# Optimization experiments

Hardware: AMD Instinct MI355X
Metric: run time of the kernel (lower is better)

## Reference

```python
import jax, jax.numpy as jnp
import numpy as np

THETA = 10000.0

def precompute_freqs_cis(dim, seq_len):
    freqs = 1.0 / THETA ** (jnp.arange(0, dim, 2)[: dim // 2].astype(jnp.float32) / dim)
    t = jnp.arange(seq_len, dtype=jnp.float32)
    ang = jnp.outer(t, freqs)  # [T, dim/2]
    return jax.lax.complex(jnp.cos(ang), jnp.sin(ang))

def apply_rope(x, freqs_cis):
    # x: [..., T, D]; freqs_cis: [T, D/2] complex
    xr = x.astype(jnp.float32).reshape(*x.shape[:-1], -1, 2)
    xc = jax.lax.complex(xr[..., 0], xr[..., 1]) * freqs_cis
    out = jnp.stack([jnp.real(xc), jnp.imag(xc)], axis=-1).reshape(x.shape)
    return out.astype(x.dtype)

def setup_inputs() -> dict:
    key = jax.random.key(0)
    k1, k2, k3, k4 = jax.random.split(key, 4)
    B, T, E, DQ, DV = 4, 2048, 1024, 128, 128
    s = 1.0 / np.sqrt(E)
    return {
        "embedding_word": jax.random.normal(k1, (B, T, E), dtype=jnp.float32),
        "w_Q": jax.random.normal(k2, (DQ, E), dtype=jnp.float32) * s,  # torch Linear weight [out,in]
        "w_K": jax.random.normal(k3, (DQ, E), dtype=jnp.float32) * s,
        "w_V": jax.random.normal(k4, (DV, E), dtype=jnp.float32) * s,
    }

def reference(embedding_word, w_Q, w_K, w_V):
    T = embedding_word.shape[-2]
    dq = w_Q.shape[0]
    q = jnp.einsum("bte,de->btd", embedding_word, w_Q)
    k = jnp.einsum("bte,de->btd", embedding_word, w_K)
    v = jnp.einsum("bte,de->btd", embedding_word, w_V)
    fc = precompute_freqs_cis(dq, T)
    q = apply_rope(q, fc)
    k = apply_rope(k, fc)
    scores = jnp.einsum("bqd,bkd->bqk", q, k)
    causal = jnp.triu(jnp.ones((T, T), dtype=bool), k=1)
    masked = jnp.where(causal, -jnp.inf, scores)
    weights = jax.nn.softmax(masked / jnp.sqrt(jnp.float32(dq)), axis=-1)
    return jnp.einsum("bqk,bkd->bqd", weights, v)
```

## Files before the change

kernel.cpp:

```cpp
#include <hip/hip_runtime.h>
#include <math.h>


#define B_ 4
#define T_ 2048
#define E_ 1024
#define D_ 128
#define BT_ (B_ * T_)

#define UNITS_PER_B 160
#define UNITS (UNITS_PER_B * B_)

typedef __bf16 bf16_t;
typedef __bf16 bf16x4 __attribute__((ext_vector_type(4)));
typedef __bf16 bf16x8 __attribute__((ext_vector_type(8)));
typedef float f32x4 __attribute__((ext_vector_type(4)));

#define GLD16(g, l)                                                         \
  __builtin_amdgcn_global_load_lds(                                         \
      (const __attribute__((address_space(1))) void*)(g),                   \
      (__attribute__((address_space(3))) void*)(l), 16, 0, 0)

__global__ __launch_bounds__(256) void precast_kernel(
    const float* __restrict__ X, const float* __restrict__ Wq,
    const float* __restrict__ Wk, const float* __restrict__ Wv,
    bf16_t* __restrict__ Xb, bf16_t* __restrict__ Wb) {
  const int XC = BT_ * E_ / 8;
  const int WC = 3 * D_ * E_ / 8;
  for (int c = blockIdx.x * 256 + threadIdx.x; c < XC + WC;
       c += gridDim.x * 256) {
    const float* src;
    bf16_t* dst;
    if (c < XC) {
      src = X + (size_t)c * 8;
      dst = Xb + (size_t)c * 8;
    } else {
      const int cw = c - XC;
      const int z = cw / (D_ * E_ / 8);
      const int r = cw % (D_ * E_ / 8);
      src = ((z == 0) ? Wq : (z == 1) ? Wk : Wv) + (size_t)r * 8;
      dst = Wb + (size_t)z * D_ * E_ + (size_t)r * 8;
    }
    float4 u = *(const float4*)src;
    float4 v = *(const float4*)(src + 4);
    bf16x8 t;
    t[0] = (bf16_t)u.x; t[1] = (bf16_t)u.y; t[2] = (bf16_t)u.z; t[3] = (bf16_t)u.w;
    t[4] = (bf16_t)v.x; t[5] = (bf16_t)v.y; t[6] = (bf16_t)v.z; t[7] = (bf16_t)v.w;
    *(bf16x8*)dst = t;
  }
}

__global__ __launch_bounds__(256) void proj64_kernel(
    const bf16_t* __restrict__ Xb, const bf16_t* __restrict__ Wb,
    bf16_t* __restrict__ Qws, bf16_t* __restrict__ Kws,
    bf16_t* __restrict__ Vtws) {
  const int o = blockIdx.x;
  const int ell = (o & 7) * 96 + (o >> 3);
  const int mt = ell / 6, ny = ell % 6;
  const int bt0 = mt * 64;

  const int tid = threadIdx.x;
  const int lane = tid & 63;
  const int wv = tid >> 6;
  const int wr = wv >> 1, wc = wv & 1;
  const int g = lane >> 4, lm = lane & 15;

  __shared__ bf16_t Ab[2][64 * 64];
  __shared__ bf16_t Bb[2][64 * 64];

  const bf16_t* Wz = Wb + (size_t)ny * 64 * E_;

  f32x4 acc[2][2];
#pragma unroll
  for (int m = 0; m < 2; m++)
#pragma unroll
    for (int n = 0; n < 2; n++) acc[m][n] = 0.0f;

  auto stage = [&](int t, int bf) {
    const int k0 = t * 64;
#pragma unroll
    for (int j = 0; j < 2; j++) {
      const int cb = (wv * 2 + j) * 64;
      const int c = cb + lane;
      const int row = c >> 3;
      const int eoff = ((c & 7) * 8) ^ ((row & 7) << 3);
      GLD16(Xb + (size_t)(bt0 + row) * E_ + k0 + eoff, &Ab[bf][cb * 8]);
    }
#pragma unroll
    for (int j = 0; j < 2; j++) {
      const int cb = (wv * 2 + j) * 64;
      const int c = cb + lane;
      const int row = c >> 3;
      const int eoff = ((c & 7) * 8) ^ ((row & 7) << 3);
      GLD16(Wz + (size_t)row * E_ + k0 + eoff, &Bb[bf][cb * 8]);
    }
  };

  auto compute = [&](int bf) {
#pragma unroll
    for (int ks = 0; ks < 2; ks++) {
      bf16x8 a0, a1, b0, b1;
      {
        const int r0 = wr * 32 + lm;
        a0 = *(const bf16x8*)&Ab[bf][r0 * 64 + ((ks * 32 + g * 8) ^ ((r0 & 7) << 3))];
        const int r1 = wr * 32 + 16 + lm;
        a1 = *(const bf16x8*)&Ab[bf][r1 * 64 + ((ks * 32 + g * 8) ^ ((r1 & 7) << 3))];
        const int s0 = wc * 32 + lm;
        b0 = *(const bf16x8*)&Bb[bf][s0 * 64 + ((ks * 32 + g * 8) ^ ((s0 & 7) << 3))];
        const int s1 = wc * 32 + 16 + lm;
        b1 = *(const bf16x8*)&Bb[bf][s1 * 64 + ((ks * 32 + g * 8) ^ ((s1 & 7) << 3))];
      }
      acc[0][0] = __builtin_amdgcn_mfma_f32_16x16x32_bf16(a0, b0, acc[0][0], 0, 0, 0);
      acc[0][1] = __builtin_amdgcn_mfma_f32_16x16x32_bf16(a0, b1, acc[0][1], 0, 0, 0);
      acc[1][0] = __builtin_amdgcn_mfma_f32_16x16x32_bf16(a1, b0, acc[1][0], 0, 0, 0);
      acc[1][1] = __builtin_amdgcn_mfma_f32_16x16x32_bf16(a1, b1, acc[1][1], 0, 0, 0);
    }
  };

  stage(0, 0);
  __syncthreads();
  int cur = 0;
  for (int t = 0; t < 16; t++) {
    if (t < 15) stage(t + 1, cur ^ 1);
    compute(cur);
    __syncthreads();
    cur ^= 1;
  }

  const float NLOG_ = -0.14391156514261485f;
  const int b = bt0 >> 11;
#pragma unroll
  for (int nf = 0; nf < 2; nf++) {
    const int col = ny * 64 + wc * 32 + nf * 16 + lm;
    const int z = col >> 7;
    const int d = col & 127;
    const float freq = expf(NLOG_ * (float)(d >> 1));
#pragma unroll
    for (int mf = 0; mf < 2; mf++) {
      const int row0 = bt0 + wr * 32 + mf * 16 + g * 4;
      if (z < 2) {
        bf16_t* dst = (z == 0) ? Qws : Kws;
#pragma unroll
        for (int r = 0; r < 4; r++) {
          const int bt = row0 + r;
          const int tt = bt & (T_ - 1);
          float val = acc[mf][nf][r];
          float prt = __shfl_xor(val, 1, 64);
          float sn, cs;
          sincosf((float)tt * freq, &sn, &cs);
          const float outv = (d & 1) ? (prt * sn + val * cs) : (val * cs - prt * sn);
          dst[(size_t)bt * D_ + d] = (bf16_t)outv;
        }
      } else {
        bf16x4 pv;
#pragma unroll
        for (int r = 0; r < 4; r++) pv[r] = (bf16_t)acc[mf][nf][r];
        const int tt0 = row0 & (T_ - 1);
        *(bf16x4*)&Vtws[((size_t)(b * D_ + d)) * T_ + tt0] = pv;
      }
    }
  }
}

__global__ __launch_bounds__(128) void attn_part_kernel(
    const bf16_t* __restrict__ Qws, const bf16_t* __restrict__ Kws,
    const bf16_t* __restrict__ Vtws, float* __restrict__ Opart,
    float* __restrict__ Mpart, float* __restrict__ Lpart) {
  const int idx = blockIdx.x;
  const int b = idx / UNITS_PER_B;
  const int rem = idx % UNITS_PER_B;
  int qi, ci;
  if (rem < 16) { qi = rem; ci = 0; }
  else if (rem < 48) { int r2 = rem - 16; qi = 16 + (r2 >> 1); ci = r2 & 1; }
  else if (rem < 96) { int r2 = rem - 48; qi = 32 + r2 / 3; ci = r2 % 3; }
  else { int r2 = rem - 96; qi = 48 + (r2 >> 2); ci = r2 & 3; }
  const int slot = idx;

  const int q0 = qi * 32;
  const int tiles = (qi >> 1) + 1;
  const int t0 = ci * 8;
  const int t1 = min(t0 + 8, tiles);

  const int tid = threadIdx.x;
  const int lane = tid & 63;
  const int wv = tid >> 6;
  const int g = lane >> 4;
  const int lm = lane & 15;

  __shared__ bf16_t Ks[64 * 136];
  __shared__ bf16_t Vts[128 * 72];
  __shared__ bf16_t Ps[2 * 16 * 72];

  bf16x8 qf[4];
  {
    const bf16_t* qb = Qws + (size_t)(b * T_ + q0 + wv * 16 + lm) * D_;
#pragma unroll
    for (int kc = 0; kc < 4; kc++) qf[kc] = *(const bf16x8*)(qb + kc * 32 + g * 8);
  }

  f32x4 o[8];
#pragma unroll
  for (int i = 0; i < 8; i++) o[i] = 0.0f;
  float m_r[4], l_r[4];
#pragma unroll
  for (int r = 0; r < 4; r++) { m_r[r] = -1e30f; l_r[r] = 0.0f; }
  const float sc = 0.08838834764831845f;

  for (int it = t0; it < t1; it++) {
    const int k0 = it * 64;
#pragma unroll
    for (int i = 0; i < 8; i++) {
      const int c = tid + i * 128;
      const int row = c >> 4, part = c & 15;
      bf16x8 v = *(const bf16x8*)(Kws + (size_t)(b * T_ + k0 + row) * D_ + part * 8);
      *(bf16x8*)&Ks[row * 136 + part * 8] = v;
    }
#pragma unroll
    for (int i = 0; i < 8; i++) {
      const int c = tid + i * 128;
      const int d = c >> 3, part = c & 7;
      bf16x8 v = *(const bf16x8*)(Vtws + (size_t)(b * D_ + d) * T_ + k0 + part * 8);
      *(bf16x8*)&Vts[d * 72 + part * 8] = v;
    }
    __syncthreads();

    f32x4 s[4];
#pragma unroll
    for (int nb = 0; nb < 4; nb++) s[nb] = 0.0f;
#pragma unroll
    for (int nb = 0; nb < 4; nb++) {
#pragma unroll
      for (int kc = 0; kc < 4; kc++) {
        bf16x8 bk = *(const bf16x8*)&Ks[(nb * 16 + lm) * 136 + kc * 32 + g * 8];
        s[nb] = __builtin_amdgcn_mfma_f32_16x16x32_bf16(qf[kc], bk, s[nb], 0, 0, 0);
      }
    }

    const bool diag = (it == tiles - 1);
#pragma unroll
    for (int r = 0; r < 4; r++) {
      const int qrow = q0 + wv * 16 + g * 4 + r;
      float sv[4];
#pragma unroll
      for (int nb = 0; nb < 4; nb++) {
        sv[nb] = s[nb][r] * sc;
        if (diag && (k0 + nb * 16 + lm > qrow)) sv[nb] = -1e30f;
      }
      float tm = fmaxf(fmaxf(sv[0], sv[1]), fmaxf(sv[2], sv[3]));
      tm = fmaxf(tm, __shfl_xor(tm, 1, 64));
      tm = fmaxf(tm, __shfl_xor(tm, 2, 64));
      tm = fmaxf(tm, __shfl_xor(tm, 4, 64));
      tm = fmaxf(tm, __shfl_xor(tm, 8, 64));
      const float mnew = fmaxf(m_r[r], tm);
      const float alpha = __expf(m_r[r] - mnew);
      float p[4], rs = 0.0f;
#pragma unroll
      for (int nb = 0; nb < 4; nb++) { p[nb] = __expf(sv[nb] - mnew); rs += p[nb]; }
      rs += __shfl_xor(rs, 1, 64);
      rs += __shfl_xor(rs, 2, 64);
      rs += __shfl_xor(rs, 4, 64);
      rs += __shfl_xor(rs, 8, 64);
      l_r[r] = l_r[r] * alpha + rs;
      m_r[r] = mnew;
#pragma unroll
      for (int nb2 = 0; nb2 < 8; nb2++) o[nb2][r] *= alpha;
#pragma unroll
      for (int nb = 0; nb < 4; nb++)
        Ps[wv * 1152 + (g * 4 + r) * 72 + nb * 16 + lm] = (bf16_t)p[nb];
    }

    bf16x8 pa0 = *(const bf16x8*)&Ps[wv * 1152 + lm * 72 + g * 8];
    bf16x8 pa1 = *(const bf16x8*)&Ps[wv * 1152 + lm * 72 + 32 + g * 8];
#pragma unroll
    for (int nb2 = 0; nb2 < 8; nb2++) {
      bf16x8 bv0 = *(const bf16x8*)&Vts[(nb2 * 16 + lm) * 72 + g * 8];
      o[nb2] = __builtin_amdgcn_mfma_f32_16x16x32_bf16(pa0, bv0, o[nb2], 0, 0, 0);
      bf16x8 bv1 = *(const bf16x8*)&Vts[(nb2 * 16 + lm) * 72 + 32 + g * 8];
      o[nb2] = __builtin_amdgcn_mfma_f32_16x16x32_bf16(pa1, bv1, o[nb2], 0, 0, 0);
    }
    __syncthreads();
  }

#pragma unroll
  for (int r = 0; r < 4; r++) {
    const int row = wv * 16 + g * 4 + r;
    if (lm == 0) {
      Mpart[slot * 32 + row] = m_r[r];
      Lpart[slot * 32 + row] = l_r[r];
    }
    float* dst = Opart + ((size_t)slot * 32 + row) * D_;
#pragma unroll
    for (int nb2 = 0; nb2 < 8; nb2++) dst[nb2 * 16 + lm] = o[nb2][r];
  }
}

__global__ __launch_bounds__(256) void attn_combine_kernel(
    const float* __restrict__ Opart, const float* __restrict__ Mpart,
    const float* __restrict__ Lpart, float* __restrict__ Out) {
  const int qi = blockIdx.x;
  const int b = blockIdx.y;
  const int gg = qi >> 4;
  const int nc = gg + 1;
  const int base = b * UNITS_PER_B + ((gg * (gg + 1)) / 2) * 16 + (qi & 15) * nc;
  const int t = threadIdx.x;
  const int row = t >> 3;
  const int d0 = (t & 7) * 16;

  float mv[4];
  float mmax = -1e30f;
  for (int ci = 0; ci < nc; ci++) {
    mv[ci] = Mpart[(base + ci) * 32 + row];
    mmax = fmaxf(mmax, mv[ci]);
  }
  f32x4 acc[4];
#pragma unroll
  for (int j = 0; j < 4; j++) acc[j] = 0.0f;
  float l = 0.0f;
  for (int ci = 0; ci < nc; ci++) {
    const float w = __expf(mv[ci] - mmax);
    l += w * Lpart[(base + ci) * 32 + row];
    const float* op = Opart + ((size_t)(base + ci) * 32 + row) * D_ + d0;
#pragma unroll
    for (int j = 0; j < 4; j++) {
      float4 v = *(const float4*)(op + j * 4);
      acc[j][0] += w * v.x; acc[j][1] += w * v.y;
      acc[j][2] += w * v.z; acc[j][3] += w * v.w;
    }
  }
  const float inv = 1.0f / l;
  float* dst = Out + ((size_t)(b * T_ + qi * 32 + row)) * D_ + d0;
#pragma unroll
  for (int j = 0; j < 4; j++) {
    float4 v;
    v.x = acc[j][0] * inv; v.y = acc[j][1] * inv;
    v.z = acc[j][2] * inv; v.w = acc[j][3] * inv;
    *(float4*)(dst + j * 4) = v;
  }
}

__global__ __launch_bounds__(256) void proj_rope_kernel(
    const float* __restrict__ X, const float* __restrict__ Wq,
    const float* __restrict__ Wk, const float* __restrict__ Wv,
    bf16_t* __restrict__ Qws, bf16_t* __restrict__ Kws,
    bf16_t* __restrict__ Vtws) {
  const int z = blockIdx.y;
  const float* __restrict__ W = (z == 0) ? Wq : (z == 1) ? Wk : Wv;
  const int bt0 = blockIdx.x * 64;
  const int tid = threadIdx.x;
  const int lane = tid & 63;
  const int wv = tid >> 6;
  const int g = lane >> 4;
  const int lm = lane & 15;

  __shared__ bf16_t Xs[64 * 40];
  __shared__ bf16_t Ws[128 * 40];

  f32x4 acc[8];
#pragma unroll
  for (int i = 0; i < 8; i++) acc[i] = 0.0f;

  for (int kk = 0; kk < E_ / 32; kk++) {
    {
      const int row = tid >> 2, c0 = (tid & 3) * 8;
      const float* src = X + (size_t)(bt0 + row) * E_ + kk * 32 + c0;
      float4 u = *(const float4*)src;
      float4 v = *(const float4*)(src + 4);
      bf16x8 t;
      t[0] = (bf16_t)u.x; t[1] = (bf16_t)u.y; t[2] = (bf16_t)u.z; t[3] = (bf16_t)u.w;
      t[4] = (bf16_t)v.x; t[5] = (bf16_t)v.y; t[6] = (bf16_t)v.z; t[7] = (bf16_t)v.w;
      *(bf16x8*)&Xs[row * 40 + c0] = t;
    }
#pragma unroll
    for (int h = 0; h < 2; h++) {
      const int cc = tid * 2 + h;
      const int row = cc >> 2, c0 = (cc & 3) * 8;
      const float* src = W + (size_t)row * E_ + kk * 32 + c0;
      float4 u = *(const float4*)src;
      float4 v = *(const float4*)(src + 4);
      bf16x8 t;
      t[0] = (bf16_t)u.x; t[1] = (bf16_t)u.y; t[2] = (bf16_t)u.z; t[3] = (bf16_t)u.w;
      t[4] = (bf16_t)v.x; t[5] = (bf16_t)v.y; t[6] = (bf16_t)v.z; t[7] = (bf16_t)v.w;
      *(bf16x8*)&Ws[row * 40 + c0] = t;
    }
    __syncthreads();
    bf16x8 a = *(const bf16x8*)&Xs[(wv * 16 + lm) * 40 + g * 8];
#pragma unroll
    for (int nb = 0; nb < 8; nb++) {
      bf16x8 bb = *(const bf16x8*)&Ws[(nb * 16 + lm) * 40 + g * 8];
      acc[nb] = __builtin_amdgcn_mfma_f32_16x16x32_bf16(a, bb, acc[nb], 0, 0, 0);
    }
    __syncthreads();
  }
  const float NLOG_ = -0.14391156514261485f;
#pragma unroll
  for (int nb = 0; nb < 8; nb++) {
    const int col = nb * 16 + lm;
    const float freq = expf(NLOG_ * (float)(col >> 1));
#pragma unroll
    for (int r = 0; r < 4; r++) {
      const int bt = bt0 + wv * 16 + g * 4 + r;
      float val = acc[nb][r];
      float prt = __shfl_xor(val, 1, 64);
      if (z < 2) {
        const int t = bt & (T_ - 1);
        const float ang = (float)t * freq;
        float sn, cs;
        sincosf(ang, &sn, &cs);
        const float outv = (col & 1) ? (prt * sn + val * cs) : (val * cs - prt * sn);
        bf16_t* dst = (z == 0) ? Qws : Kws;
        dst[(size_t)bt * D_ + col] = (bf16_t)outv;
      } else {
        const int b = bt >> 11, t = bt & (T_ - 1);
        Vtws[((size_t)(b * D_ + col)) * T_ + t] = (bf16_t)val;
      }
    }
  }
}

__global__ __launch_bounds__(128) void attn_kernel(
    const bf16_t* __restrict__ Qws, const bf16_t* __restrict__ Kws,
    const bf16_t* __restrict__ Vtws, float* __restrict__ Out) {
  const int b = blockIdx.y;
  const int qi = blockIdx.x;
  const int q0 = qi * 32;
  const int tid = threadIdx.x;
  const int lane = tid & 63;
  const int wv = tid >> 6;
  const int g = lane >> 4;
  const int lm = lane & 15;

  __shared__ bf16_t Ks[32 * 136];
  __shared__ bf16_t Vts[128 * 40];
  __shared__ bf16_t Ps[2 * 16 * 40];

  bf16x8 qf[4];
  {
    const bf16_t* qb = Qws + (size_t)(b * T_ + q0 + wv * 16 + lm) * D_;
#pragma unroll
    for (int kk = 0; kk < 4; kk++) qf[kk] = *(const bf16x8*)(qb + kk * 32 + g * 8);
  }
  f32x4 o[8];
#pragma unroll
  for (int i = 0; i < 8; i++) o[i] = 0.0f;
  float m_r[4], l_r[4];
#pragma unroll
  for (int r = 0; r < 4; r++) { m_r[r] = -1e30f; l_r[r] = 0.0f; }
  const float sc = 0.08838834764831845f;

  for (int kt = 0; kt <= qi; kt++) {
    const int kv0 = kt * 32;
#pragma unroll
    for (int i = 0; i < 4; i++) {
      const int c = tid + i * 128;
      const int row = c >> 4, part = c & 15;
      bf16x8 v = *(const bf16x8*)(Kws + (size_t)(b * T_ + kv0 + row) * D_ + part * 8);
      *(bf16x8*)&Ks[row * 136 + part * 8] = v;
    }
#pragma unroll
    for (int i = 0; i < 4; i++) {
      const int c = tid + i * 128;
      const int d = c >> 2, part = c & 3;
      bf16x8 v = *(const bf16x8*)(Vtws + (size_t)(b * D_ + d) * T_ + kv0 + part * 8);
      *(bf16x8*)&Vts[d * 40 + part * 8] = v;
    }
    __syncthreads();
    f32x4 s[2];
    s[0] = 0.0f; s[1] = 0.0f;
#pragma unroll
    for (int nb = 0; nb < 2; nb++) {
#pragma unroll
      for (int kc = 0; kc < 4; kc++) {
        bf16x8 bk = *(const bf16x8*)&Ks[(nb * 16 + lm) * 136 + kc * 32 + g * 8];
        s[nb] = __builtin_amdgcn_mfma_f32_16x16x32_bf16(qf[kc], bk, s[nb], 0, 0, 0);
      }
    }
    const bool diag = (kt == qi);
#pragma unroll
    for (int r = 0; r < 4; r++) {
      float sv0 = s[0][r] * sc;
      float sv1 = s[1][r] * sc;
      if (diag) {
        const int rowr = wv * 16 + g * 4 + r;
        if (lm > rowr) sv0 = -1e30f;
        if (lm + 16 > rowr) sv1 = -1e30f;
      }
      float tm = fmaxf(sv0, sv1);
      tm = fmaxf(tm, __shfl_xor(tm, 1, 64));
      tm = fmaxf(tm, __shfl_xor(tm, 2, 64));
      tm = fmaxf(tm, __shfl_xor(tm, 4, 64));
      tm = fmaxf(tm, __shfl_xor(tm, 8, 64));
      const float mnew = fmaxf(m_r[r], tm);
      const float alpha = __expf(m_r[r] - mnew);
      const float p0 = __expf(sv0 - mnew);
      const float p1 = __expf(sv1 - mnew);
      float rs = p0 + p1;
      rs += __shfl_xor(rs, 1, 64);
      rs += __shfl_xor(rs, 2, 64);
      rs += __shfl_xor(rs, 4, 64);
      rs += __shfl_xor(rs, 8, 64);
      l_r[r] = l_r[r] * alpha + rs;
      m_r[r] = mnew;
#pragma unroll
      for (int nb2 = 0; nb2 < 8; nb2++) o[nb2][r] *= alpha;
      Ps[wv * 640 + (g * 4 + r) * 40 + lm] = (bf16_t)p0;
      Ps[wv * 640 + (g * 4 + r) * 40 + 16 + lm] = (bf16_t)p1;
    }
    bf16x8 pa = *(const bf16x8*)&Ps[wv * 640 + lm * 40 + g * 8];
#pragma unroll
    for (int nb2 = 0; nb2 < 8; nb2++) {
      bf16x8 bv = *(const bf16x8*)&Vts[(nb2 * 16 + lm) * 40 + g * 8];
      o[nb2] = __builtin_amdgcn_mfma_f32_16x16x32_bf16(pa, bv, o[nb2], 0, 0, 0);
    }
    __syncthreads();
  }
#pragma unroll
  for (int r = 0; r < 4; r++) {
    const float inv = 1.0f / l_r[r];
    float* dst = Out + (size_t)(b * T_ + q0 + wv * 16 + g * 4 + r) * D_;
#pragma unroll
    for (int nb2 = 0; nb2 < 8; nb2++) dst[nb2 * 16 + lm] = o[nb2][r] * inv;
  }
}

extern "C" void kernel_launch(void* const* d_in, const int* in_sizes, int n_in,
                              void* d_out, int out_size, void* d_ws,
                              size_t ws_size, hipStream_t stream) {
  const float* X = (const float*)d_in[0];
  const float* Wq = (const float*)d_in[1];
  const float* Wk = (const float*)d_in[2];
  const float* Wv = (const float*)d_in[3];
  float* Out = (float*)d_out;

  const size_t xb_bytes = (size_t)BT_ * E_ * sizeof(bf16_t);
  const size_t wb_bytes = (size_t)3 * D_ * E_ * sizeof(bf16_t);
  const size_t qkv_bytes = (size_t)3 * BT_ * D_ * sizeof(bf16_t);
  const size_t opart_bytes = (size_t)UNITS * 32 * D_ * sizeof(float);
  const size_t ml_bytes = (size_t)UNITS * 32 * sizeof(float);

  const size_t needA = xb_bytes + wb_bytes + qkv_bytes + opart_bytes + 2 * ml_bytes;
  const size_t needB = qkv_bytes + opart_bytes + 2 * ml_bytes;

  if (ws_size >= needA) {
    bf16_t* Xb = (bf16_t*)d_ws;
    bf16_t* Wb = Xb + (size_t)BT_ * E_;
    bf16_t* Qws = Wb + (size_t)3 * D_ * E_;
    bf16_t* Kws = Qws + (size_t)BT_ * D_;
    bf16_t* Vtws = Kws + (size_t)BT_ * D_;
    float* Opart = (float*)((char*)d_ws + xb_bytes + wb_bytes + qkv_bytes);
    float* Mpart = (float*)((char*)Opart + opart_bytes);
    float* Lpart = (float*)((char*)Mpart + ml_bytes);

    hipLaunchKernelGGL(precast_kernel, dim3(2048), dim3(256), 0, stream,
                       X, Wq, Wk, Wv, Xb, Wb);
    hipLaunchKernelGGL(proj64_kernel, dim3(768), dim3(256), 0, stream,
                       Xb, Wb, Qws, Kws, Vtws);
    hipLaunchKernelGGL(attn_part_kernel, dim3(UNITS), dim3(128), 0, stream,
                       Qws, Kws, Vtws, Opart, Mpart, Lpart);
    hipLaunchKernelGGL(attn_combine_kernel, dim3(T_ / 32, B_), dim3(256), 0,
                       stream, Opart, Mpart, Lpart, Out);
  } else if (ws_size >= needB) {
    bf16_t* Qws = (bf16_t*)d_ws;
    bf16_t* Kws = Qws + (size_t)BT_ * D_;
    bf16_t* Vtws = Kws + (size_t)BT_ * D_;
    float* Opart = (float*)((char*)d_ws + qkv_bytes);
    float* Mpart = (float*)((char*)Opart + opart_bytes);
    float* Lpart = (float*)((char*)Mpart + ml_bytes);
    hipLaunchKernelGGL(proj_rope_kernel, dim3(BT_ / 64, 3), dim3(256), 0,
                       stream, X, Wq, Wk, Wv, Qws, Kws, Vtws);
    hipLaunchKernelGGL(attn_part_kernel, dim3(UNITS), dim3(128), 0, stream,
                       Qws, Kws, Vtws, Opart, Mpart, Lpart);
    hipLaunchKernelGGL(attn_combine_kernel, dim3(T_ / 32, B_), dim3(256), 0,
                       stream, Opart, Mpart, Lpart, Out);
  } else {
    bf16_t* Qws = (bf16_t*)d_ws;
    bf16_t* Kws = Qws + (size_t)BT_ * D_;
    bf16_t* Vtws = Kws + (size_t)BT_ * D_;
    hipLaunchKernelGGL(proj_rope_kernel, dim3(BT_ / 64, 3), dim3(256), 0,
                       stream, X, Wq, Wk, Wv, Qws, Kws, Vtws);
    hipLaunchKernelGGL(attn_kernel, dim3(T_ / 32, B_), dim3(128), 0, stream,
                       Qws, Kws, Vtws, Out);
  }
}
```

Measured before the change: 71.82 us.

## Prefetch next K/V tile into registers and precompute RoPE cos/sin table

The attention kernel now loads the next K and V tiles from global memory into registers while the current tile is computed, then writes them to LDS at the top of the next iteration, so global latency overlaps MFMA work. Separately, the RoPE sin/cos values are computed once into a workspace table inside the precast kernel and read in the projection epilogue, replacing per-element sincosf/expf calls. The prefetch adds 16 bf16x8 registers per thread, which can reduce occupancy. The table adds a 1 MB workspace buffer and extra global reads in the epilogue.

```diff
diff --git a/kernel.cpp b/kernel.cpp
--- a/kernel.cpp
+++ b/kernel.cpp
@@ -24,7 +24,8 @@
 __global__ __launch_bounds__(256) void precast_kernel(
     const float* __restrict__ X, const float* __restrict__ Wq,
     const float* __restrict__ Wk, const float* __restrict__ Wv,
-    bf16_t* __restrict__ Xb, bf16_t* __restrict__ Wb) {
+    bf16_t* __restrict__ Xb, bf16_t* __restrict__ Wb,
+    float2* __restrict__ Tab) {
   const int XC = BT_ * E_ / 8;
   const int WC = 3 * D_ * E_ / 8;
   for (int c = blockIdx.x * 256 + threadIdx.x; c < XC + WC;
@@ -48,12 +49,21 @@
     t[4] = (bf16_t)v.x; t[5] = (bf16_t)v.y; t[6] = (bf16_t)v.z; t[7] = (bf16_t)v.w;
     *(bf16x8*)dst = t;
   }
+  const float NLOG_ = -0.14391156514261485f;
+  for (int idx = blockIdx.x * 256 + threadIdx.x; idx < T_ * 64;
+       idx += gridDim.x * 256) {
+    const int t = idx >> 6, j = idx & 63;
+    const float freq = expf(NLOG_ * (float)j);
+    float sn, cs;
+    sincosf((float)t * freq, &sn, &cs);
+    Tab[idx] = make_float2(cs, sn);
+  }
 }
 
 __global__ __launch_bounds__(256) void proj64_kernel(
     const bf16_t* __restrict__ Xb, const bf16_t* __restrict__ Wb,
-    bf16_t* __restrict__ Qws, bf16_t* __restrict__ Kws,
-    bf16_t* __restrict__ Vtws) {
+    const float2* __restrict__ Tab, bf16_t* __restrict__ Qws,
+    bf16_t* __restrict__ Kws, bf16_t* __restrict__ Vtws) {
   const int o = blockIdx.x;
   const int ell = (o & 7) * 96 + (o >> 3);
   const int mt = ell / 6, ny = ell % 6;
@@ -127,14 +137,12 @@
     cur ^= 1;
   }
 
-  const float NLOG_ = -0.14391156514261485f;
   const int b = bt0 >> 11;
 #pragma unroll
   for (int nf = 0; nf < 2; nf++) {
     const int col = ny * 64 + wc * 32 + nf * 16 + lm;
     const int z = col >> 7;
     const int d = col & 127;
-    const float freq = expf(NLOG_ * (float)(d >> 1));
 #pragma unroll
     for (int mf = 0; mf < 2; mf++) {
       const int row0 = bt0 + wr * 32 + mf * 16 + g * 4;
@@ -146,9 +154,9 @@
           const int tt = bt & (T_ - 1);
           float val = acc[mf][nf][r];
           float prt = __shfl_xor(val, 1, 64);
-          float sn, cs;
-          sincosf((float)tt * freq, &sn, &cs);
-          const float outv = (d & 1) ? (prt * sn + val * cs) : (val * cs - prt * sn);
+          const float2 cs = Tab[(size_t)tt * 64 + (d >> 1)];
+          const float outv =
+              (d & 1) ? (prt * cs.y + val * cs.x) : (val * cs.x - prt * cs.y);
           dst[(size_t)bt * D_ + d] = (bf16_t)outv;
         }
       } else {
@@ -206,24 +214,42 @@
   for (int r = 0; r < 4; r++) { m_r[r] = -1e30f; l_r[r] = 0.0f; }
   const float sc = 0.08838834764831845f;
 
-  for (int it = t0; it < t1; it++) {
+  bf16x8 kreg[8], vreg[8];
+  auto load_tiles = [&](int it) {
     const int k0 = it * 64;
 #pragma unroll
     for (int i = 0; i < 8; i++) {
       const int c = tid + i * 128;
-      const int row = c >> 4, part = c & 15;
-      bf16x8 v = *(const bf16x8*)(Kws + (size_t)(b * T_ + k0 + row) * D_ + part * 8);
-      *(bf16x8*)&Ks[row * 136 + part * 8] = v;
+      kreg[i] = *(const bf16x8*)(Kws + (size_t)(b * T_ + k0 + (c >> 4)) * D_ +
+                                 (c & 15) * 8);
     }
 #pragma unroll
     for (int i = 0; i < 8; i++) {
       const int c = tid + i * 128;
-      const int d = c >> 3, part = c & 7;
-      bf16x8 v = *(const bf16x8*)(Vtws + (size_t)(b * D_ + d) * T_ + k0 + part * 8);
-      *(bf16x8*)&Vts[d * 72 + part * 8] = v;
-    }
+      vreg[i] = *(const bf16x8*)(Vtws + (size_t)(b * D_ + (c >> 3)) * T_ + k0 +
+                                 (c & 7) * 8);
+    }
+  };
+  auto write_lds = [&]() {
+#pragma unroll
+    for (int i = 0; i < 8; i++) {
+      const int c = tid + i * 128;
+      *(bf16x8*)&Ks[(c >> 4) * 136 + (c & 15) * 8] = kreg[i];
+    }
+#pragma unroll
+    for (int i = 0; i < 8; i++) {
+      const int c = tid + i * 128;
+      *(bf16x8*)&Vts[(c >> 3) * 72 + (c & 7) * 8] = vreg[i];
+    }
+  };
+
+  load_tiles(t0);
+  for (int it = t0; it < t1; it++) {
+    write_lds();
     __syncthreads();
-
+    if (it + 1 < t1) load_tiles(it + 1);
+
+    const int k0 = it * 64;
     f32x4 s[4];
 #pragma unroll
     for (int nb = 0; nb < 4; nb++) s[nb] = 0.0f;
@@ -536,8 +562,10 @@
   const size_t qkv_bytes = (size_t)3 * BT_ * D_ * sizeof(bf16_t);
   const size_t opart_bytes = (size_t)UNITS * 32 * D_ * sizeof(float);
   const size_t ml_bytes = (size_t)UNITS * 32 * sizeof(float);
-
-  const size_t needA = xb_bytes + wb_bytes + qkv_bytes + opart_bytes + 2 * ml_bytes;
+  const size_t tab_bytes = (size_t)T_ * 64 * sizeof(float2);
+
+  const size_t needA =
+      xb_bytes + wb_bytes + qkv_bytes + opart_bytes + 2 * ml_bytes + tab_bytes;
   const size_t needB = qkv_bytes + opart_bytes + 2 * ml_bytes;
 
   if (ws_size >= needA) {
@@ -549,11 +577,12 @@
     float* Opart = (float*)((char*)d_ws + xb_bytes + wb_bytes + qkv_bytes);
     float* Mpart = (float*)((char*)Opart + opart_bytes);
     float* Lpart = (float*)((char*)Mpart + ml_bytes);
+    float2* Tab = (float2*)((char*)Lpart + ml_bytes);
 
     hipLaunchKernelGGL(precast_kernel, dim3(2048), dim3(256), 0, stream,
-                       X, Wq, Wk, Wv, Xb, Wb);
+                       X, Wq, Wk, Wv, Xb, Wb, Tab);
     hipLaunchKernelGGL(proj64_kernel, dim3(768), dim3(256), 0, stream,
-                       Xb, Wb, Qws, Kws, Vtws);
+                       Xb, Wb, Tab, Qws, Kws, Vtws);
     hipLaunchKernelGGL(attn_part_kernel, dim3(UNITS), dim3(128), 0, stream,
                        Qws, Kws, Vtws, Opart, Mpart, Lpart);
     hipLaunchKernelGGL(attn_combine_kernel, dim3(T_ / 32, B_), dim3(256), 0,
```

After: 62.42 us. 1.15x faster.
